# Kernel tuning notes

Measured on AMD Instinct MI355X. Metric: run time of the kernel, lower is better.

The kernel has to match this reference:

```python
import jax, jax.numpy as jnp
import numpy as np

B, N, D, H = 8, 1024, 768, 12
HD = D // H  # head_dim = 64


def setup_inputs() -> dict:
    key = jax.random.key(0)
    k1, k2 = jax.random.split(key)
    x = jax.random.normal(k1, (B, N, D), dtype=jnp.float32)
    W_qkv = jax.random.normal(k2, (D, 3 * D), dtype=jnp.float32) * 0.02
    b_qkv = jnp.zeros((3 * D,), dtype=jnp.float32)
    return {"x": x, "W_qkv": W_qkv, "b_qkv": b_qkv}


def reference(x, W_qkv, b_qkv):
    b, n, d = x.shape
    qkv = x @ W_qkv + b_qkv                      # [B, N, 3D]
    qkv = qkv.reshape(b, n, 3, H, HD)
    qkv = jnp.transpose(qkv, (2, 0, 3, 1, 4))    # [3, B, H, N, HD]
    q, k, v = qkv[0], qkv[1], qkv[2]
    scale = 1.0 / jnp.sqrt(jnp.float32(HD))
    scores = jnp.einsum('bhqd,bhkd->bhqk', q, k) * scale   # [B, H, N, N]
    attn = jax.nn.softmax(scores, axis=-1)
    out = jnp.einsum('bhqk,bhkd->bhqd', attn, v)            # [B, H, N, HD]
    # concat heads along last dim (same as torch.cat over head outputs)
    return jnp.transpose(out, (0, 2, 1, 3)).reshape(b, n, d)
```

## Files before the change

### kernel.cpp

```cpp
#include <hip/hip_runtime.h>
#include <stdint.h>

#define BB 8
#define NN 1024
#define DDIM 768
#define HH 12
#define HDIM 64
#define D3 2304
#define MM 8192

typedef __attribute__((ext_vector_type(4))) float f32x4;
typedef __attribute__((ext_vector_type(16))) float f32x16;
typedef __attribute__((ext_vector_type(8))) __bf16 bf16x8;
typedef __attribute__((ext_vector_type(8))) unsigned short u16x8;
typedef __attribute__((ext_vector_type(4))) unsigned short u16x4;

__device__ __forceinline__ unsigned short f2bf(float f) {
  unsigned int u = __float_as_uint(f);
  u += 0x7FFFu + ((u >> 16) & 1u);
  return (unsigned short)(u >> 16);
}

__device__ __forceinline__ void gload_lds16(const void* g, void* l) {
  __builtin_amdgcn_global_load_lds((const __attribute__((address_space(1))) void*)g,
                                   (__attribute__((address_space(3))) void*)l,
                                   16, 0, 0);
}

__device__ __forceinline__ unsigned cvtpk_bf16(float lo, float hi) {
  unsigned r;
  asm("v_cvt_pk_bf16_f32 %0, %1, %2" : "=v"(r) : "v"(lo), "v"(hi));
  return r;
}

__device__ __forceinline__ bf16x8 mkfrag(unsigned a, unsigned b, unsigned c, unsigned d) {
  union { unsigned u[4]; bf16x8 v; } x;
  x.u[0] = a; x.u[1] = b; x.u[2] = c; x.u[3] = d;
  return x.v;
}

#if __has_builtin(__builtin_amdgcn_exp2f)
#define EXP2(x) __builtin_amdgcn_exp2f(x)
#else
#define EXP2(x) exp2f(x)
#endif

#define QSCL 0.18033688f

__global__ void k_prep(const float4* __restrict__ x, u16x4* __restrict__ xb,
                       const float* __restrict__ W, unsigned short* __restrict__ Wt) {
  __shared__ float tile[32][33];
  const int bid = blockIdx.x;
  if (bid < 6144) {
    int i = bid * 256 + threadIdx.x;
    float4 v = x[i];
    u16x4 o;
    o[0] = f2bf(v.x); o[1] = f2bf(v.y); o[2] = f2bf(v.z); o[3] = f2bf(v.w);
    xb[i] = o;
    return;
  }
  const int bid2 = bid - 6144;
  const int tx = threadIdx.x & 31, ty = threadIdx.x >> 5;
  const int n0 = (bid2 % 72) * 32;
  const int k0 = (bid2 / 72) * 32;
  for (int i = 0; i < 4; ++i) {
    int k = k0 + ty + i * 8;
    tile[ty + i * 8][tx] = W[(size_t)k * D3 + n0 + tx];
  }
  __syncthreads();
  for (int i = 0; i < 4; ++i) {
    int n = n0 + ty + i * 8;
    Wt[(size_t)n * DDIM + k0 + tx] = f2bf(tile[tx][ty + i * 8]);
  }
}

__global__ __launch_bounds__(256, 3)
void k_gemm(const unsigned short* __restrict__ A, const unsigned short* __restrict__ Bt,
            const float* __restrict__ bias, unsigned short* __restrict__ qb,
            unsigned short* __restrict__ kp, unsigned short* __restrict__ vp) {
  __shared__ char lds[48 * 1024];
  const int t = threadIdx.x, lane = t & 63, wid = t >> 6;
  const int orig = blockIdx.x;
  const int xcd = orig & 7, tt = orig >> 3;
  const int m0 = (xcd * 8 + (tt & 7)) * 128;
  const int n0 = (tt >> 3) * 128;
  const int wr = wid >> 1, wc = wid & 1;
  const int grp = lane >> 4, lc = lane & 15;

  f32x4 acc[4][4];
  for (int i = 0; i < 4; ++i)
    for (int j = 0; j < 4; ++j) acc[i][j] = (f32x4)(0.0f);

  auto STAGE = [&](int buf, int kt) {
    char* Ab = lds + buf * 16384;
    char* Bb = Ab + 8192;
#pragma unroll
    for (int i = 0; i < 2; ++i) {
      int chunk = wid * 2 + i;
      int g = chunk * 64 + lane;
      int row = g >> 2, c16 = (g & 3) << 4;
      gload_lds16((const char*)A + (size_t)(m0 + row) * 1536 + kt * 64 + c16, Ab + chunk * 1024);
      gload_lds16((const char*)Bt + (size_t)(n0 + row) * 1536 + kt * 64 + c16, Bb + chunk * 1024);
    }
  };

  STAGE(0, 0);
  asm volatile("s_waitcnt vmcnt(0)" ::: "memory");
  __builtin_amdgcn_s_barrier();

  int cur = 0;
  for (int kt = 0; kt < 24; ++kt) {
    const int nxt = (cur == 2) ? 0 : cur + 1;
    if (kt < 23) {
      STAGE(nxt, kt + 1);
      asm volatile("s_waitcnt vmcnt(4)" ::: "memory");
    } else {
      asm volatile("s_waitcnt vmcnt(0)" ::: "memory");
    }
    __builtin_amdgcn_s_barrier();

    const char* As = lds + cur * 16384;
    const char* Bs = As + 8192;
    bf16x8 af[4], bfr[4];
#pragma unroll
    for (int f = 0; f < 4; ++f) {
      af[f]  = *(const bf16x8*)(As + (wr * 64 + f * 16 + lc) * 64 + grp * 16);
      bfr[f] = *(const bf16x8*)(Bs + (wc * 64 + f * 16 + lc) * 64 + grp * 16);
    }
    __builtin_amdgcn_s_setprio(1);
#pragma unroll
    for (int mf = 0; mf < 4; ++mf)
#pragma unroll
      for (int nf = 0; nf < 4; ++nf)
        acc[mf][nf] = __builtin_amdgcn_mfma_f32_16x16x32_bf16(af[mf], bfr[nf], acc[mf][nf], 0, 0, 0);
    __builtin_amdgcn_s_setprio(0);
    cur = nxt;
  }

  float bv[4];
#pragma unroll
  for (int nf = 0; nf < 4; ++nf) bv[nf] = bias[n0 + wc * 64 + nf * 16 + lc];

  const int nt = n0 >> 7;
  if (nt < 6) {
#pragma unroll
    for (int mf = 0; mf < 4; ++mf)
#pragma unroll
      for (int nf = 0; nf < 4; ++nf)
#pragma unroll
        for (int i = 0; i < 4; ++i) {
          int r = m0 + wr * 64 + mf * 16 + grp * 4 + i;
          int c = n0 + wc * 64 + nf * 16 + lc;
          qb[(size_t)r * DDIM + c] = f2bf((acc[mf][nf][i] + bv[nf]) * QSCL);
        }
  } else {
    __syncthreads();
    unsigned short* lt = (unsigned short*)lds + wid * 4608;
    const int l31 = lane & 31, hi2 = lane >> 5;
    const int bb = m0 >> 10;
    const int kt_ = ((m0 & 1023) >> 6) + wr;
    size_t base;
    unsigned short* dst;
    if (nt < 12) {
      const int h = ((n0 - DDIM) >> 6) + wc;
      base = ((size_t)(bb * HH + h) * 16 + kt_) * 4096;
      dst = kp;
#pragma unroll
      for (int mf = 0; mf < 4; ++mf)
#pragma unroll
        for (int nf = 0; nf < 4; ++nf)
#pragma unroll
          for (int i = 0; i < 4; ++i)
            lt[(mf * 16 + grp * 4 + i) * 72 + nf * 16 + lc] = f2bf(acc[mf][nf][i] + bv[nf]);
    } else {
      const int h = ((n0 - 2 * DDIM) >> 6) + wc;
      base = ((size_t)(bb * HH + h) * 16 + kt_) * 4096;
      dst = vp;
#pragma unroll
      for (int mf = 0; mf < 4; ++mf)
#pragma unroll
        for (int nf = 0; nf < 4; ++nf)
#pragma unroll
          for (int i = 0; i < 4; ++i)
            lt[(nf * 16 + lc) * 72 + mf * 16 + grp * 4 + i] = f2bf(acc[mf][nf][i] + bv[nf]);
    }
    __syncthreads();
#pragma unroll
    for (int c2 = 0; c2 < 4; ++c2)
#pragma unroll
      for (int r = 0; r < 2; ++r)
        *(u16x8*)(dst + base + ((size_t)(c2 * 2 + r) * 64 + lane) * 8) =
          *(const u16x8*)&lt[(r * 32 + l31) * 72 + c2 * 16 + hi2 * 8];
  }
}

__global__ __launch_bounds__(256, 3)
void k_attn(const unsigned short* __restrict__ qb,
            const unsigned short* __restrict__ kp, const unsigned short* __restrict__ vp,
            float* __restrict__ out) {
  __shared__ char lds[48 * 1024];
  const int lane = threadIdx.x & 63, wid = threadIdx.x >> 6;
  const int orig = blockIdx.x;
  const int wg = (orig & 7) * 96 + (orig >> 3);
  const int bh = wg >> 3, qt = wg & 7;
  const int b = bh / HH, h = bh % HH;
  const int q0 = qt * 128 + wid * 32;
  const int l31 = lane & 31, hi = lane >> 5;

  auto STAGE = [&](int bi, int kt2) {
    char* buf = lds + bi * 16384;
    const char* gk = (const char*)kp + (size_t)(bh * 16 + kt2) * 8192 + lane * 16;
    const char* gv = (const char*)vp + (size_t)(bh * 16 + kt2) * 8192 + lane * 16;
#pragma unroll
    for (int i = 0; i < 4; ++i) {
      int e = wid * 4 + i;
      const char* g = (e < 8) ? (gk + e * 1024) : (gv + (e - 8) * 1024);
      char* l = (e < 8) ? (buf + e * 1024) : (buf + 8192 + (e - 8) * 1024);
      gload_lds16(g, l);
    }
  };

  bf16x8 qf[4];
  const char* qbase = (const char*)qb + ((size_t)(b * NN + q0 + l31) * DDIM + h * HDIM) * 2;
#pragma unroll
  for (int ds_ = 0; ds_ < 4; ++ds_)
    qf[ds_] = *(const bf16x8*)(qbase + ds_ * 32 + hi * 16);

  STAGE(0, 0);
  STAGE(1, 1);

  f32x16 acc0 = (f32x16)(0.0f), acc1 = (f32x16)(0.0f);
  float l = 0.0f;

  int cur = 0;
  for (int kt = 0; kt < 16; ++kt) {
    if (kt < 15) {
      asm volatile("s_waitcnt vmcnt(4)" ::: "memory");
    } else {
      asm volatile("s_waitcnt vmcnt(0)" ::: "memory");
    }
    __builtin_amdgcn_s_barrier();
    if (kt + 2 < 16) {
      int nx = cur + 2; if (nx >= 3) nx -= 3;
      STAGE(nx, kt + 2);
    }

    const char* Kc = lds + cur * 16384;
    const char* Vc = Kc + 8192;

    bf16x8 kf[4][2];
#pragma unroll
    for (int ds_ = 0; ds_ < 4; ++ds_)
#pragma unroll
      for (int r = 0; r < 2; ++r)
        kf[ds_][r] = *(const bf16x8*)(Kc + (ds_ * 2 + r) * 1024 + lane * 16);

    f32x16 st0 = (f32x16)(0.0f), st1 = (f32x16)(0.0f);
    __builtin_amdgcn_s_setprio(1);
#pragma unroll
    for (int ds_ = 0; ds_ < 4; ++ds_) {
      st0 = __builtin_amdgcn_mfma_f32_32x32x16_bf16(kf[ds_][0], qf[ds_], st0, 0, 0, 0);
      st1 = __builtin_amdgcn_mfma_f32_32x32x16_bf16(kf[ds_][1], qf[ds_], st1, 0, 0, 0);
    }
    __builtin_amdgcn_s_setprio(0);

    bf16x8 vf[4][2];
#pragma unroll
    for (int cc = 0; cc < 4; ++cc)
#pragma unroll
      for (int r = 0; r < 2; ++r)
        vf[cc][r] = *(const bf16x8*)(Vc + (cc * 2 + r) * 1024 + lane * 16);

    float s0 = 0.f, s1 = 0.f, s2 = 0.f, s3 = 0.f;
#pragma unroll
    for (int i = 0; i < 16; i += 4) {
      float p0 = EXP2(st0[i]);
      float p1 = EXP2(st0[i + 1]);
      float p2 = EXP2(st0[i + 2]);
      float p3 = EXP2(st0[i + 3]);
      st0[i] = p0; st0[i + 1] = p1; st0[i + 2] = p2; st0[i + 3] = p3;
      s0 += p0; s1 += p1; s2 += p2; s3 += p3;
    }
#pragma unroll
    for (int i = 0; i < 16; i += 4) {
      float p0 = EXP2(st1[i]);
      float p1 = EXP2(st1[i + 1]);
      float p2 = EXP2(st1[i + 2]);
      float p3 = EXP2(st1[i + 3]);
      st1[i] = p0; st1[i + 1] = p1; st1[i + 2] = p2; st1[i + 3] = p3;
      s0 += p0; s1 += p1; s2 += p2; s3 += p3;
    }
    l += (s0 + s1) + (s2 + s3);

#pragma unroll
    for (int kblk = 0; kblk < 2; ++kblk) {
      const f32x16& sp = kblk ? st1 : st0;
      unsigned c0 = cvtpk_bf16(sp[0], sp[1]),   c1 = cvtpk_bf16(sp[2], sp[3]);
      unsigned c2 = cvtpk_bf16(sp[4], sp[5]),   c3 = cvtpk_bf16(sp[6], sp[7]);
      unsigned c4 = cvtpk_bf16(sp[8], sp[9]),   c5 = cvtpk_bf16(sp[10], sp[11]);
      unsigned c6 = cvtpk_bf16(sp[12], sp[13]), c7 = cvtpk_bf16(sp[14], sp[15]);
      unsigned z0 = hi ? c0 : c2, z1 = hi ? c1 : c3;
      unsigned z2 = hi ? c4 : c6, z3 = hi ? c5 : c7;
      unsigned w0 = __shfl_xor(z0, 32, 64), w1 = __shfl_xor(z1, 32, 64);
      unsigned w2 = __shfl_xor(z2, 32, 64), w3 = __shfl_xor(z3, 32, 64);
      bf16x8 pf0 = mkfrag(hi ? w0 : c0, hi ? w1 : c1, hi ? c2 : w0, hi ? c3 : w1);
      bf16x8 pf1 = mkfrag(hi ? w2 : c4, hi ? w3 : c5, hi ? c6 : w2, hi ? c7 : w3);

      __builtin_amdgcn_s_setprio(1);
#pragma unroll
      for (int ch = 0; ch < 2; ++ch) {
        const int cc = kblk * 2 + ch;
        const bf16x8 pf = ch ? pf1 : pf0;
        acc0 = __builtin_amdgcn_mfma_f32_32x32x16_bf16(vf[cc][0], pf, acc0, 0, 0, 0);
        acc1 = __builtin_amdgcn_mfma_f32_32x32x16_bf16(vf[cc][1], pf, acc1, 0, 0, 0);
      }
      __builtin_amdgcn_s_setprio(0);
    }

    cur = (cur == 2) ? 0 : cur + 1;
  }

  float lf = l + __shfl_xor(l, 32, 64);
  float inv = 1.0f / lf;
  float* obase = out + (size_t)(b * NN + q0 + l31) * DDIM + h * HDIM + hi * 4;
#pragma unroll
  for (int rq = 0; rq < 4; ++rq) {
    f32x4 o;
    o[0] = acc0[rq * 4] * inv; o[1] = acc0[rq * 4 + 1] * inv;
    o[2] = acc0[rq * 4 + 2] * inv; o[3] = acc0[rq * 4 + 3] * inv;
    *(f32x4*)(obase + rq * 8) = o;
  }
#pragma unroll
  for (int rq = 0; rq < 4; ++rq) {
    f32x4 o;
    o[0] = acc1[rq * 4] * inv; o[1] = acc1[rq * 4 + 1] * inv;
    o[2] = acc1[rq * 4 + 2] * inv; o[3] = acc1[rq * 4 + 3] * inv;
    *(f32x4*)(obase + 32 + rq * 8) = o;
  }
}

extern "C" void kernel_launch(void* const* d_in, const int* in_sizes, int n_in,
                              void* d_out, int out_size, void* d_ws, size_t ws_size,
                              hipStream_t stream) {
  const float* x = (const float*)d_in[0];
  const float* W = (const float*)d_in[1];
  const float* bqkv = (const float*)d_in[2];
  float* out = (float*)d_out;
  char* ws = (char*)d_ws;

  const size_t XB_OFF = 0;
  const size_t WT_OFF = 12582912;
  const size_t QB_OFF = WT_OFF + 3538944;
  const size_t KP_OFF = QB_OFF + 12582912;
  const size_t VP_OFF = KP_OFF + 12582912;
  unsigned short* xb = (unsigned short*)(ws + XB_OFF);
  unsigned short* wt = (unsigned short*)(ws + WT_OFF);
  unsigned short* qbf = (unsigned short*)(ws + QB_OFF);
  unsigned short* kpk = (unsigned short*)(ws + KP_OFF);
  unsigned short* vpk = (unsigned short*)(ws + VP_OFF);

  k_prep<<<dim3(6144 + 1728), dim3(256), 0, stream>>>((const float4*)x, (u16x4*)xb, W, wt);
  k_gemm<<<dim3(1152), dim3(256), 0, stream>>>(xb, wt, bqkv, qbf, kpk, vpk);
  k_attn<<<dim3(768), dim3(256), 0, stream>>>(qbf, kpk, vpk, out);
}
```

Measured before the change: 87.76 us.

## Double K-step GEMM tile to 64 with XOR-swizzled LDS and double buffering

Widens the QKV projection GEMM's K tile from 32 to 64 bf16 elements, halving the number of main-loop iterations and barriers. It replaces triple buffering with double buffering plus a trailing barrier, and XOR-swizzles the LDS column layout so the wider rows avoid bank conflicts. LDS per block grows to 64KB and the launch-bounds occupancy hint drops from 3 to 2 blocks, trading occupancy and one level of prefetch depth for fewer synchronizations and more MFMA work per barrier.

```diff
diff --git a/kernel.cpp b/kernel.cpp
--- a/kernel.cpp
+++ b/kernel.cpp
@@ -74,11 +74,11 @@
   }
 }
 
-__global__ __launch_bounds__(256, 3)
+__global__ __launch_bounds__(256, 2)
 void k_gemm(const unsigned short* __restrict__ A, const unsigned short* __restrict__ Bt,
             const float* __restrict__ bias, unsigned short* __restrict__ qb,
             unsigned short* __restrict__ kp, unsigned short* __restrict__ vp) {
-  __shared__ char lds[48 * 1024];
+  __shared__ char lds[64 * 1024];
   const int t = threadIdx.x, lane = t & 63, wid = t >> 6;
   const int orig = blockIdx.x;
   const int xcd = orig & 7, tt = orig >> 3;
@@ -92,49 +92,50 @@
     for (int j = 0; j < 4; ++j) acc[i][j] = (f32x4)(0.0f);
 
   auto STAGE = [&](int buf, int kt) {
-    char* Ab = lds + buf * 16384;
-    char* Bb = Ab + 8192;
-#pragma unroll
-    for (int i = 0; i < 2; ++i) {
-      int chunk = wid * 2 + i;
-      int g = chunk * 64 + lane;
-      int row = g >> 2, c16 = (g & 3) << 4;
-      gload_lds16((const char*)A + (size_t)(m0 + row) * 1536 + kt * 64 + c16, Ab + chunk * 1024);
-      gload_lds16((const char*)Bt + (size_t)(n0 + row) * 1536 + kt * 64 + c16, Bb + chunk * 1024);
+    char* Ab = lds + buf * 32768;
+    char* Bb = Ab + 16384;
+#pragma unroll
+    for (int i = 0; i < 4; ++i) {
+      int id = wid * 4 + i;
+      int row = id * 8 + (lane >> 3);
+      int cs = ((lane & 7) << 4) ^ ((row & 7) << 4);
+      gload_lds16((const char*)A + (size_t)(m0 + row) * 1536 + kt * 128 + cs, Ab + id * 1024);
+      gload_lds16((const char*)Bt + (size_t)(n0 + row) * 1536 + kt * 128 + cs, Bb + id * 1024);
     }
   };
 
   STAGE(0, 0);
-  asm volatile("s_waitcnt vmcnt(0)" ::: "memory");
-  __builtin_amdgcn_s_barrier();
-
-  int cur = 0;
-  for (int kt = 0; kt < 24; ++kt) {
-    const int nxt = (cur == 2) ? 0 : cur + 1;
-    if (kt < 23) {
-      STAGE(nxt, kt + 1);
-      asm volatile("s_waitcnt vmcnt(4)" ::: "memory");
+  for (int kt = 0; kt < 12; ++kt) {
+    if (kt < 11) {
+      STAGE((kt + 1) & 1, kt + 1);
+      asm volatile("s_waitcnt vmcnt(8)" ::: "memory");
     } else {
       asm volatile("s_waitcnt vmcnt(0)" ::: "memory");
     }
     __builtin_amdgcn_s_barrier();
 
-    const char* As = lds + cur * 16384;
-    const char* Bs = As + 8192;
-    bf16x8 af[4], bfr[4];
-#pragma unroll
-    for (int f = 0; f < 4; ++f) {
-      af[f]  = *(const bf16x8*)(As + (wr * 64 + f * 16 + lc) * 64 + grp * 16);
-      bfr[f] = *(const bf16x8*)(Bs + (wc * 64 + f * 16 + lc) * 64 + grp * 16);
-    }
+    const char* As = lds + (kt & 1) * 32768;
+    const char* Bs = As + 16384;
+    bf16x8 af[4][2], bfr[4][2];
+#pragma unroll
+    for (int f = 0; f < 4; ++f)
+#pragma unroll
+      for (int kk = 0; kk < 2; ++kk) {
+        int ra = wr * 64 + f * 16 + lc;
+        af[f][kk] = *(const bf16x8*)(As + ra * 128 + ((kk * 64 + grp * 16) ^ ((ra & 7) << 4)));
+        int rb = wc * 64 + f * 16 + lc;
+        bfr[f][kk] = *(const bf16x8*)(Bs + rb * 128 + ((kk * 64 + grp * 16) ^ ((rb & 7) << 4)));
+      }
     __builtin_amdgcn_s_setprio(1);
 #pragma unroll
     for (int mf = 0; mf < 4; ++mf)
 #pragma unroll
-      for (int nf = 0; nf < 4; ++nf)
-        acc[mf][nf] = __builtin_amdgcn_mfma_f32_16x16x32_bf16(af[mf], bfr[nf], acc[mf][nf], 0, 0, 0);
+      for (int nf = 0; nf < 4; ++nf) {
+        acc[mf][nf] = __builtin_amdgcn_mfma_f32_16x16x32_bf16(af[mf][0], bfr[nf][0], acc[mf][nf], 0, 0, 0);
+        acc[mf][nf] = __builtin_amdgcn_mfma_f32_16x16x32_bf16(af[mf][1], bfr[nf][1], acc[mf][nf], 0, 0, 0);
+      }
     __builtin_amdgcn_s_setprio(0);
-    cur = nxt;
+    __builtin_amdgcn_s_barrier();
   }
 
   float bv[4];
```

Result: faster. 82.37 us (median of 4 runs) (-6.1%).
